# Performance work log

Hardware: AMD Instinct MI355X
Metric: run time of the kernel (lower is better)

The kernel has to match this reference:

```python
import jax, jax.numpy as jnp
import numpy as np

B, D_IN, FD = 32768, 2048, 128
N1 = N2 = N3 = 4
T = 1.0  # temperature buffer value (eval mode)
LN_EPS = 1e-5

def _gelu(x):
    return jax.nn.gelu(x, approximate=False)  # torch nn.GELU default = exact erf

def setup_inputs() -> dict:
    key = jax.random.key(0)
    ks = iter(jax.random.split(key, 64))
    def rn(shape, s=0.02):
        return jax.random.normal(next(ks), shape, jnp.float32) * s
    inp = {"x": jax.random.normal(next(ks), (B, D_IN), jnp.float32)}
    # input_proj: Linear(2048,512) GELU Linear(512,256) LayerNorm(256)
    inp.update(ipW1=rn((D_IN, 512)), ipb1=jnp.zeros(512), ipW2=rn((512, 256)), ipb2=jnp.zeros(256),
               ln_g=jnp.ones(256), ln_b=jnp.zeros(256))
    def level(din, nc, pfx):
        return {pfx+"W3d": rn((din, 3)), pfx+"b3d": jnp.zeros(3),
                pfx+"c": rn((nc, 3), 0.3), pfx+"lr": jnp.zeros(nc),
                pfx+"f1W": rn((din, FD)), pfx+"f1b": jnp.zeros(FD),
                pfx+"f2W": rn((FD, FD)), pfx+"f2b": jnp.zeros(FD),
                pfx+"rW": rn((FD+3, nc)), pfx+"rb": jnp.zeros(nc)}
    inp.update(level(256, N1, "l1"))
    inp.update(level(FD, N2, "l2"))
    inp.update(level(FD, N3, "l3"))
    # expert_head: Linear(128+4+4+4, 256) GELU Linear(256, 64)
    inp.update(ehW1=rn((FD+N1+N2+N3, 256)), ehb1=jnp.zeros(256),
               ehW2=rn((256, N1*N2*N3)), ehb2=jnp.zeros(N1*N2*N3))
    return inp

def _level_fwd(x, W3d, b3d, c, f1W, f1b, f2W, f2b, rW, rb):
    # x: (B, din) -> probs (B, nc), features (B, FD)
    pos = x @ W3d + b3d                                   # (B, 3)
    d_sq = ((pos[:, None, :] - c[None, :, :]) ** 2).sum(-1)  # (B, nc)
    geo = -d_sq / (2.0 * T * T + 1e-8)                    # non-spectral geo signal
    feat = _gelu(x @ f1W + f1b) @ f2W + f2b               # (B, FD)
    logits = jnp.concatenate([feat, pos], axis=-1) @ rW + rb + 0.5 * geo
    probs = jax.nn.softmax(logits / max(T, 0.1), axis=-1)  # eval path: plain softmax
    return probs, feat

def _router_fwd(x, ipW1, ipb1, ipW2, ipb2, ln_g, ln_b,
                l1W3d, l1b3d, l1c, l1f1W, l1f1b, l1f2W, l1f2b, l1rW, l1rb,
                l2W3d, l2b3d, l2c, l2f1W, l2f1b, l2f2W, l2f2b, l2rW, l2rb,
                l3W3d, l3b3d, l3c, l3f1W, l3f1b, l3f2W, l3f2b, l3rW, l3rb,
                ehW1, ehb1, ehW2, ehb2):
    h = _gelu(x @ ipW1 + ipb1) @ ipW2 + ipb2
    mu = h.mean(-1, keepdims=True)
    var = ((h - mu) ** 2).mean(-1, keepdims=True)
    h = (h - mu) * jax.lax.rsqrt(var + LN_EPS) * ln_g + ln_b  # LayerNorm(256)
    p1, f1 = _level_fwd(h,  l1W3d, l1b3d, l1c, l1f1W, l1f1b, l1f2W, l1f2b, l1rW, l1rb)
    p2, f2 = _level_fwd(f1, l2W3d, l2b3d, l2c, l2f1W, l2f1b, l2f2W, l2f2b, l2rW, l2rb)
    p3, f3 = _level_fwd(f2, l3W3d, l3b3d, l3c, l3f1W, l3f1b, l3f2W, l3f2b, l3rW, l3rb)
    combined = jnp.concatenate([f3, p1, p2, p3], axis=-1)  # (B, 140)
    logits = _gelu(combined @ ehW1 + ehb1) @ ehW2 + ehb2   # (B, 64)
    expert_probs = jax.nn.softmax(logits / max(T, 0.1), axis=-1)
    return expert_probs

def reference(x, ipW1, ipb1, ipW2, ipb2, ln_g, ln_b,
              l1W3d, l1b3d, l1c, l1lr, l1f1W, l1f1b, l1f2W, l1f2b, l1rW, l1rb,
              l2W3d, l2b3d, l2c, l2lr, l2f1W, l2f1b, l2f2W, l2f2b, l2rW, l2rb,
              l3W3d, l3b3d, l3c, l3lr, l3f1W, l3f1b, l3f2W, l3f2b, l3rW, l3rb,
              ehW1, ehb1, ehW2, ehb2):
    # l?lr (log_radii) are unused in non-spectral mode, matching the source.
    expert_probs = _router_fwd(x, ipW1, ipb1, ipW2, ipb2, ln_g, ln_b,
                               l1W3d, l1b3d, l1c, l1f1W, l1f1b, l1f2W, l1f2b, l1rW, l1rb,
                               l2W3d, l2b3d, l2c, l2f1W, l2f1b, l2f2W, l2f2b, l2rW, l2rb,
                               l3W3d, l3b3d, l3c, l3f1W, l3f1b, l3f2W, l3f2b, l3rW, l3rb,
                               ehW1, ehb1, ehW2, ehb2)
    expert_ids = jnp.argmax(expert_probs, axis=-1)
    return expert_probs, expert_ids
```

## Files before the change

kernel.cpp:

```cpp
#include <hip/hip_runtime.h>
#include <hip/hip_bf16.h>
#include <cstdint>
#include <cstddef>


typedef short  s8v  __attribute__((ext_vector_type(8)));
typedef float  f4v  __attribute__((ext_vector_type(4)));
typedef float  f16v __attribute__((ext_vector_type(16)));
typedef unsigned int u32;

#define B_ROWS 32768

__device__ inline short f2bf(float x) {
    __hip_bfloat16 h = __float2bfloat16(x);
    return __builtin_bit_cast(short, h);
}
__device__ inline float bf2f(short s) {
    return __bfloat162float(__builtin_bit_cast(__hip_bfloat16, s));
}
__device__ inline float gelu_f(float x) {
    return 0.5f * x * (1.0f + erff(x * 0.70710678118654752440f));
}
__device__ inline void gload_lds16(const short* g, short* l) {
    __builtin_amdgcn_global_load_lds(
        (const __attribute__((address_space(1))) u32*)g,
        (__attribute__((address_space(3))) u32*)l, 16, 0, 0);
}

__global__ void split_w1_img(const float* __restrict__ W, short* __restrict__ img)
{
    const int idx = blockIdx.x * 256 + threadIdx.x;
    const int p = idx & 7;
    const int n = (idx >> 3) & 511;
    const int t = idx >> 12;
    const int cs = p ^ (n & 7);
    const int plane = cs >> 2, kc = cs & 3;
    const int kbase = t * 32 + kc * 8;
    s8v v8;
    #pragma unroll
    for (int e = 0; e < 8; ++e) {
        const float v = W[(size_t)(kbase + e) * 512 + n];
        const short h = f2bf(v);
        v8[e] = plane ? f2bf(v - bf2f(h)) : h;
    }
    *(s8v*)&img[(size_t)((t * 512 + n) * 64 + p * 8)] = v8;
}

__launch_bounds__(256, 4)
__global__ void gemm1k(const float* __restrict__ X,
                       const short* __restrict__ Bimg,
                       const float* __restrict__ bias,
                       float* __restrict__ out)
{
    __shared__ short smem[128 * 64 * 2];
    short* Ab = smem;
    short* Bb = smem + 128 * 64;

    const int tid = threadIdx.x;
    const int l = tid & 63, wid = tid >> 6;
    const int wr = wid >> 1, wc = wid & 1;

    const int d = blockIdx.x;
    const int xcd = d & 7;
    const int m0 = ((xcd & 1) * 128 + (d >> 3)) * 128;
    const int n0 = (xcd >> 1) * 128;

    const int ar = tid & 127, ah = tid >> 7;
    const float* xP = X + (size_t)(m0 + ar) * 2048 + ah * 16;
    short* awr = Ab + ar * 64;
    const int pw0 = ((ah * 2    ) ^ (ar & 7)) * 8;
    const int pw1 = ((ah * 2 + 1) ^ (ar & 7)) * 8;
    const int pw2 = ((ah * 2 + 4) ^ (ar & 7)) * 8;
    const int pw3 = ((ah * 2 + 5) ^ (ar & 7)) * 8;

    const short* bP = Bimg + (size_t)n0 * 64 + (size_t)(wid * 4) * 512 + (size_t)l * 8;
    short* bD = Bb + wid * 4 * 512;

    f16v acc[2][2];
    #pragma unroll
    for (int m = 0; m < 2; ++m)
        #pragma unroll
        for (int n = 0; n < 2; ++n) acc[m][n] = (f16v)0.0f;

    f4v cur0, cur1, cur2, cur3;
    cur0 = *(const f4v*)(xP + 0);
    cur1 = *(const f4v*)(xP + 4);
    cur2 = *(const f4v*)(xP + 8);
    cur3 = *(const f4v*)(xP + 12);

    for (int t = 0; t < 64; ++t) {
        s8v hi0, hi1, lo0, lo1;
        #pragma unroll
        for (int e = 0; e < 4; ++e) {
            float v;
            short h;
            v = cur0[e]; h = f2bf(v); hi0[e]     = h; lo0[e]     = f2bf(v - bf2f(h));
            v = cur1[e]; h = f2bf(v); hi0[e + 4] = h; lo0[e + 4] = f2bf(v - bf2f(h));
            v = cur2[e]; h = f2bf(v); hi1[e]     = h; lo1[e]     = f2bf(v - bf2f(h));
            v = cur3[e]; h = f2bf(v); hi1[e + 4] = h; lo1[e + 4] = f2bf(v - bf2f(h));
        }
        __syncthreads();
        *(s8v*)&awr[pw0] = hi0;
        *(s8v*)&awr[pw1] = hi1;
        *(s8v*)&awr[pw2] = lo0;
        *(s8v*)&awr[pw3] = lo1;
        {
            const short* bt = bP + (size_t)t * 32768;
            gload_lds16(bt,          bD);
            gload_lds16(bt +  512,   bD + 512);
            gload_lds16(bt + 1024,   bD + 1024);
            gload_lds16(bt + 1536,   bD + 1536);
        }
        if (t < 63) {
            const float* p = xP + (t + 1) * 32;
            cur0 = *(const f4v*)(p + 0);
            cur1 = *(const f4v*)(p + 4);
            cur2 = *(const f4v*)(p + 8);
            cur3 = *(const f4v*)(p + 12);
        }
        __syncthreads();

        #pragma unroll
        for (int ks = 0; ks < 2; ++ks) {
            const int ph = (ks * 2 + (l >> 5)) ^ (l & 7);
            s8v ahf[2], alf[2], bhf[2], blf[2];
            #pragma unroll
            for (int m = 0; m < 2; ++m) {
                const int row = wr * 64 + m * 32 + (l & 31);
                ahf[m] = *(const s8v*)&Ab[row * 64 + ph * 8];
                alf[m] = *(const s8v*)&Ab[row * 64 + (ph ^ 4) * 8];
            }
            #pragma unroll
            for (int n = 0; n < 2; ++n) {
                const int col = wc * 64 + n * 32 + (l & 31);
                bhf[n] = *(const s8v*)&Bb[col * 64 + ph * 8];
                blf[n] = *(const s8v*)&Bb[col * 64 + (ph ^ 4) * 8];
            }
            #pragma unroll
            for (int m = 0; m < 2; ++m)
                #pragma unroll
                for (int n = 0; n < 2; ++n) {
                    acc[m][n] = __builtin_amdgcn_mfma_f32_32x32x16_bf16(ahf[m], bhf[n], acc[m][n], 0, 0, 0);
                    acc[m][n] = __builtin_amdgcn_mfma_f32_32x32x16_bf16(ahf[m], blf[n], acc[m][n], 0, 0, 0);
                    acc[m][n] = __builtin_amdgcn_mfma_f32_32x32x16_bf16(alf[m], bhf[n], acc[m][n], 0, 0, 0);
                }
        }
    }

    #pragma unroll
    for (int m = 0; m < 2; ++m) {
        #pragma unroll
        for (int n = 0; n < 2; ++n) {
            const int gcol = n0 + wc * 64 + n * 32 + (l & 31);
            const float bv = bias[gcol];
            #pragma unroll
            for (int r = 0; r < 16; ++r) {
                const int grow = m0 + wr * 64 + m * 32
                               + (r & 3) + 8 * (r >> 2) + 4 * (l >> 5);
                out[(size_t)grow * 512 + gcol] = gelu_f(acc[m][n][r] + bv);
            }
        }
    }
}

struct SplitDesc { const float* W; short* dst; int K, N, Kpad, blk0; };
struct SplitPack { SplitDesc d[9]; };

__global__ void split_all(SplitPack p) {
    const int bid = blockIdx.x;
    int i = 0;
    #pragma unroll
    for (int j = 1; j < 9; ++j) if (bid >= p.d[j].blk0) i = j;
    const SplitDesc& D = p.d[i];
    const int idx = (bid - D.blk0) * 256 + threadIdx.x;
    const int total = D.N * D.Kpad;
    if (idx >= total) return;
    const int n = idx / D.Kpad, k = idx - n * D.Kpad;
    const float v = (k < D.K) ? D.W[(size_t)k * D.N + n] : 0.0f;
    const short hs = f2bf(v);
    D.dst[idx] = hs;
    D.dst[total + idx] = f2bf(v - bf2f(hs));
}

template<int BM, int BN, int EPI>
__launch_bounds__(256, 2)
__global__ void gemm32(const float* __restrict__ A, int lda,
                       const short* __restrict__ Bsp, int ldb, int NK,
                       const float* __restrict__ bias, int K, int N, int ntiles,
                       float* __restrict__ out, float* __restrict__ out2)
{
    constexpr int MF  = BM / 64;
    constexpr int NFw = BN / 64;
    constexpr int BUF = (BM + BN) * 64;
    constexpr int FPT = BM / 8;
    constexpr int TPR = 32 / FPT;
    constexpr int nBI = BN / 32;
    __shared__ short smem[2 * BUF];

    const int tid = threadIdx.x;
    const int l   = tid & 63, wid = tid >> 6;
    const int wr  = wid >> 1, wc = wid & 1;
    const int bid = blockIdx.x;
    const int ntb = bid % ntiles, mtb = bid / ntiles;
    const int m0  = mtb * BM, n0 = ntb * BN;

    const int ar = tid / TPR, aseg = tid % TPR;
    const float* aP = A + (size_t)(m0 + ar) * lda + aseg * FPT;

    const short* bg[nBI];
    {
        const int cs = (l & 7) ^ (l >> 3);
        const int plane = cs >> 2, kslot = cs & 3;
        #pragma unroll
        for (int j = 0; j < nBI; ++j) {
            const int col = (wid * nBI + j) * 8 + (l >> 3);
            bg[j] = Bsp + (size_t)plane * NK + (size_t)(n0 + col) * ldb + kslot * 8;
        }
    }

    f16v acc[MF][NFw];
    #pragma unroll
    for (int m = 0; m < MF; ++m)
// ... 58 lines not shown
                }
            __builtin_amdgcn_s_setprio(0);
        }
    };

    const int NT = K / 32;
    loadA(0);
    stageB(0, smem);
    writeA(smem);
    __syncthreads();
    for (int t = 0; t < NT; ++t) {
        short* curb = smem + (t & 1) * BUF;
        short* nxtb = smem + ((t & 1) ^ 1) * BUF;
        const bool pf = (t + 1 < NT);
        if (pf) { loadA(t + 1); stageB(t + 1, nxtb); }
        compute(curb);
        if (pf) writeA(nxtb);
        __syncthreads();
    }

    if constexpr (EPI <= 1) {
        #pragma unroll
        for (int m = 0; m < MF; ++m) {
            #pragma unroll
            for (int n = 0; n < NFw; ++n) {
                const int gcol = n0 + wc * (BN / 2) + n * 32 + (l & 31);
                const float bv = bias[gcol];
                #pragma unroll
                for (int r = 0; r < 16; ++r) {
                    const int grow = m0 + wr * (BM / 2) + m * 32
                                   + (r & 3) + 8 * (r >> 2) + 4 * (l >> 5);
                    float xv = acc[m][n][r] + bv;
                    if constexpr (EPI == 0) xv = gelu_f(xv);
                    out[(size_t)grow * N + gcol] = xv;
                }
            }
        }
    } else {
        float* LT = reinterpret_cast<float*>(smem);
        const int gcolL = wc * 32 + (l & 31);
        const float bv = bias[gcolL];
        #pragma unroll
        for (int r = 0; r < 16; ++r) {
            const int row = wr * 32 + (r & 3) + 8 * (r >> 2) + 4 * (l >> 5);
            LT[row * 64 + gcolL] = acc[0][0][r] + bv;
        }
        __syncthreads();
        const int r = tid >> 2, q = tid & 3;
        const float* Lr = LT + r * 64 + q * 16;
        float mx = Lr[0];
        #pragma unroll
        for (int c = 1; c < 16; ++c) mx = fmaxf(mx, Lr[c]);
        mx = fmaxf(mx, __shfl_xor(mx, 1));
        mx = fmaxf(mx, __shfl_xor(mx, 2));
        float ev[16]; float s = 0.0f;
        #pragma unroll
        for (int c = 0; c < 16; ++c) { ev[c] = expf(Lr[c] - mx); s += ev[c]; }
        s += __shfl_xor(s, 1);
        s += __shfl_xor(s, 2);
        float pmax = -1.0f; int arg = 0;
        #pragma unroll
        for (int c = 0; c < 16; ++c) {
            const float pv = ev[c] / s;
            out[(size_t)(m0 + r) * 64 + q * 16 + c] = pv;
            if (pv > pmax) { pmax = pv; arg = q * 16 + c; }
        }
        #pragma unroll
        for (int off = 1; off <= 2; off <<= 1) {
            const float po = __shfl_xor(pmax, off);
            const int   ao = __shfl_xor(arg, off);
            if (po > pmax || (po == pmax && ao < arg)) { pmax = po; arg = ao; }
        }
        if (q == 0) out2[m0 + r] = (float)arg;
    }
}

__global__ __launch_bounds__(256) void ln_kernel(float* __restrict__ H,
                                                 const float* __restrict__ G,
                                                 const float* __restrict__ Bv)
{
    const int row = blockIdx.x * 4 + (threadIdx.x >> 6);
    const int l   = threadIdx.x & 63;
    float* hr = H + (size_t)row * 256;
    f4v v = *reinterpret_cast<const f4v*>(&hr[l * 4]);
    float s = v[0] + v[1] + v[2] + v[3];
    #pragma unroll
    for (int o = 32; o; o >>= 1) s += __shfl_xor(s, o);
    const float mu = s * 0.00390625f;
    f4v d = v - mu;
    float q = d[0]*d[0] + d[1]*d[1] + d[2]*d[2] + d[3]*d[3];
    #pragma unroll
    for (int o = 32; o; o >>= 1) q += __shfl_xor(q, o);
    const float var = q * 0.00390625f;
    const float sc  = 1.0f / sqrtf(var + 1e-5f);
    f4v gg = *reinterpret_cast<const f4v*>(&G[l * 4]);
    f4v bb = *reinterpret_cast<const f4v*>(&Bv[l * 4]);
    f4v o4 = d * sc * gg + bb;
    *reinterpret_cast<f4v*>(&hr[l * 4]) = o4;
}

__global__ __launch_bounds__(256) void p_kernel(
    const float* __restrict__ X, int din,
    const float* __restrict__ F,
    const float* __restrict__ W3d, const float* __restrict__ b3d,
    const float* __restrict__ cc,
    const float* __restrict__ rW, const float* __restrict__ rb,
    float* __restrict__ P)
{
    const int row = blockIdx.x * 4 + (threadIdx.x >> 6);
    const int l   = threadIdx.x & 63;
    float px0 = 0.f, px1 = 0.f, px2 = 0.f;
    const int per = din >> 6;
    const float* xr = X + (size_t)row * din;
    for (int i = 0; i < per; ++i) {
        const int k = l + (i << 6);
        const float xv = xr[k];
        px0 += xv * W3d[k*3 + 0];
        px1 += xv * W3d[k*3 + 1];
        px2 += xv * W3d[k*3 + 2];
    }
    float g0 = 0.f, g1 = 0.f, g2 = 0.f, g3 = 0.f;
    const float* fr = F + (size_t)row * 128;
    #pragma unroll
    for (int i = 0; i < 2; ++i) {
        const int k = l + (i << 6);
        const float fv = fr[k];
        g0 += fv * rW[k*4 + 0]; g1 += fv * rW[k*4 + 1];
        g2 += fv * rW[k*4 + 2]; g3 += fv * rW[k*4 + 3];
    }
    #pragma unroll
    for (int o = 32; o; o >>= 1) {
        px0 += __shfl_xor(px0, o); px1 += __shfl_xor(px1, o); px2 += __shfl_xor(px2, o);
        g0  += __shfl_xor(g0, o);  g1  += __shfl_xor(g1, o);
        g2  += __shfl_xor(g2, o);  g3  += __shfl_xor(g3, o);
    }
    if (l == 0) {
        const float pos0 = px0 + b3d[0], pos1 = px1 + b3d[1], pos2 = px2 + b3d[2];
        float lg[4];
        float mx = -1e30f;
        float gg[4] = {g0, g1, g2, g3};
        #pragma unroll
        for (int c = 0; c < 4; ++c) {
            float a = gg[c] + rb[c]
                    + pos0 * rW[512 + c] + pos1 * rW[516 + c] + pos2 * rW[520 + c];
            const float d0 = pos0 - cc[c*3 + 0];
            const float d1 = pos1 - cc[c*3 + 1];
            const float d2 = pos2 - cc[c*3 + 2];
            a += 0.5f * (-(d0*d0 + d1*d1 + d2*d2) / 2.00000001f);
            lg[c] = a;
            mx = fmaxf(mx, a);
        }
        const float e0 = expf(lg[0]-mx), e1 = expf(lg[1]-mx),
                    e2 = expf(lg[2]-mx), e3 = expf(lg[3]-mx);
        const float s = e0 + e1 + e2 + e3;
        float* pr = P + (size_t)row * 4;
        pr[0] = e0/s; pr[1] = e1/s; pr[2] = e2/s; pr[3] = e3/s;
    }
}

__global__ void concat_kernel(const float* __restrict__ f3,
                              const float* __restrict__ P1,
                              const float* __restrict__ P2,
                              const float* __restrict__ P3,
                              float* __restrict__ C)
{
    const int idx = blockIdx.x * 256 + threadIdx.x;
    const int row = idx / 160, j = idx - row * 160;
    float v;
    if      (j < 128) v = f3[(size_t)row * 128 + j];
    else if (j < 132) v = P1[(size_t)row * 4 + (j - 128)];
    else if (j < 136) v = P2[(size_t)row * 4 + (j - 132)];
    else if (j < 140) v = P3[(size_t)row * 4 + (j - 136)];
    else              v = 0.0f;
    C[idx] = v;
}

extern "C" void kernel_launch(void* const* d_in, const int* in_sizes, int n_in,
                              void* d_out, int out_size, void* d_ws, size_t ws_size,
                              hipStream_t stream)
{
    (void)in_sizes; (void)n_in; (void)out_size; (void)ws_size;

    const float* x    = (const float*)d_in[0];
    const float* ipW1 = (const float*)d_in[1];
    const float* ipb1 = (const float*)d_in[2];
    const float* ipW2 = (const float*)d_in[3];
    const float* ipb2 = (const float*)d_in[4];
    const float* ln_g = (const float*)d_in[5];
    const float* ln_b = (const float*)d_in[6];
    const float* W3d[3] = {(const float*)d_in[7],  (const float*)d_in[17], (const float*)d_in[27]};
    const float* b3d[3] = {(const float*)d_in[8],  (const float*)d_in[18], (const float*)d_in[28]};
    const float* cc[3]  = {(const float*)d_in[9],  (const float*)d_in[19], (const float*)d_in[29]};
    const float* f1W[3] = {(const float*)d_in[11], (const float*)d_in[21], (const float*)d_in[31]};
    const float* f1b[3] = {(const float*)d_in[12], (const float*)d_in[22], (const float*)d_in[32]};
    const float* f2W[3] = {(const float*)d_in[13], (const float*)d_in[23], (const float*)d_in[33]};
    const float* f2b[3] = {(const float*)d_in[14], (const float*)d_in[24], (const float*)d_in[34]};
    const float* rW[3]  = {(const float*)d_in[15], (const float*)d_in[25], (const float*)d_in[35]};
    const float* rb[3]  = {(const float*)d_in[16], (const float*)d_in[26], (const float*)d_in[36]};
    const float* ehW1 = (const float*)d_in[37];
    const float* ehb1 = (const float*)d_in[38];
    const float* ehW2 = (const float*)d_in[39];
    const float* ehb2 = (const float*)d_in[40];

    size_t off = 0;
    auto take = [&](size_t bytes) -> void* {
        void* p = (char*)d_ws + off;
        off += (bytes + 255) & ~(size_t)255;
        return p;
    };
    auto takeW = [&](int N, int Kpad) -> short* {
        return (short*)take((size_t)2 * N * Kpad * 2);
    };
    short* W1img = (short*)take((size_t)64 * 512 * 64 * 2);
    short* W2s = takeW(256, 512);
    short* L1a = takeW(128, 256);
    short* L1b = takeW(128, 128);
    short* L2a = takeW(128, 128);
    short* L2b = takeW(128, 128);
    short* L3a = takeW(128, 128);
    short* L3b = takeW(128, 128);
    short* E1s = takeW(256, 160);
    short* E2s = takeW(64, 256);
    float* h1 = (float*)take((size_t)B_ROWS * 512 * 4);
    float* h2 = (float*)take((size_t)B_ROWS * 256 * 4);
    float* zg = (float*)take((size_t)B_ROWS * 128 * 4);
    float* f1 = (float*)take((size_t)B_ROWS * 128 * 4);
    float* f2 = (float*)take((size_t)B_ROWS * 128 * 4);
    float* f3 = (float*)take((size_t)B_ROWS * 128 * 4);
    float* p1 = (float*)take((size_t)B_ROWS * 4 * 4);
    float* p2 = (float*)take((size_t)B_ROWS * 4 * 4);
    float* p3 = (float*)take((size_t)B_ROWS * 4 * 4);
    float* comb = h1;
    float* geh  = (float*)((char*)h1 + ((size_t)22 << 20));

    split_w1_img<<<(64 * 512 * 8) / 256, 256, 0, stream>>>(ipW1, W1img);
    SplitPack sp;
    int blk = 0;
    auto desc = [&](int i, const float* W, short* dst, int K, int N, int Kpad) {
        sp.d[i] = {W, dst, K, N, Kpad, blk};
        blk += (N * Kpad + 255) / 256;
    };
    desc(0, ipW2,   W2s,  512, 256,  512);
    desc(1, f1W[0], L1a,  256, 128,  256);
    desc(2, f2W[0], L1b,  128, 128,  128);
    desc(3, f1W[1], L2a,  128, 128,  128);
    desc(4, f2W[1], L2b,  128, 128,  128);
    desc(5, f1W[2], L3a,  128, 128,  128);
    desc(6, f2W[2], L3b,  128, 128,  128);
    desc(7, ehW1,   E1s,  140, 256,  160);
    desc(8, ehW2,   E2s,  256,  64,  256);
    split_all<<<blk, 256, 0, stream>>>(sp);

    const dim3 blkT(256);
    constexpr int MG128 = B_ROWS / 128;
    constexpr int MG64  = B_ROWS / 64;

    gemm1k<<<1024, blkT, 0, stream>>>(x, W1img, ipb1, h1);
    gemm32<128,128,1><<<MG128*2, blkT, 0, stream>>>(h1,  512, W2s,  512, 256*512,  ipb2,  512, 256, 2, h2, nullptr);
    ln_kernel<<<B_ROWS/4, 256, 0, stream>>>(h2, ln_g, ln_b);

    gemm32<64,128,0><<<MG64, blkT, 0, stream>>>(h2, 256, L1a, 256, 128*256, f1b[0], 256, 128, 1, zg, nullptr);
    gemm32<64,128,1><<<MG64, blkT, 0, stream>>>(zg, 128, L1b, 128, 128*128, f2b[0], 128, 128, 1, f1, nullptr);
    p_kernel<<<B_ROWS/4, 256, 0, stream>>>(h2, 256, f1, W3d[0], b3d[0], cc[0], rW[0], rb[0], p1);

    gemm32<64,128,0><<<MG64, blkT, 0, stream>>>(f1, 128, L2a, 128, 128*128, f1b[1], 128, 128, 1, zg, nullptr);
    gemm32<64,128,1><<<MG64, blkT, 0, stream>>>(zg, 128, L2b, 128, 128*128, f2b[1], 128, 128, 1, f2, nullptr);
    p_kernel<<<B_ROWS/4, 256, 0, stream>>>(f1, 128, f2, W3d[1], b3d[1], cc[1], rW[1], rb[1], p2);

    gemm32<64,128,0><<<MG64, blkT, 0, stream>>>(f2, 128, L3a, 128, 128*128, f1b[2], 128, 128, 1, zg, nullptr);
    gemm32<64,128,1><<<MG64, blkT, 0, stream>>>(zg, 128, L3b, 128, 128*128, f2b[2], 128, 128, 1, f3, nullptr);
    p_kernel<<<B_ROWS/4, 256, 0, stream>>>(f2, 128, f3, W3d[2], b3d[2], cc[2], rW[2], rb[2], p3);

    concat_kernel<<<(B_ROWS*160)/256, 256, 0, stream>>>(f3, p1, p2, p3, comb);
    gemm32<64,128,0><<<MG64*2, blkT, 0, stream>>>(comb, 160, E1s, 160, 256*160, ehb1, 160, 256, 2, geh, nullptr);
    gemm32<64,64,2><<<MG64, blkT, 0, stream>>>(geh, 256, E2s, 256, 64*256, ehb2, 256, 64, 1,
                                               (float*)d_out, (float*)d_out + (size_t)B_ROWS * 64);
}
```

Measured before the change: 495.0 us.

## Rewrite first GEMM with 256x256 tiles, double-buffered LDS and prefetch pipeline

Replaces the 128x128-tile, 256-thread first-layer GEMM with a 512-thread, 256x256-tile kernel. It double-buffers A and B in 128KB of dynamic LDS and loads the X tile two steps ahead, so global loads and the bf16 hi/lo split overlap the MFMA work. It also raises wave priority around the MFMA block and changes the block-to-XCD mapping. The larger tile improves data reuse and cuts the barrier per step, at the cost of one block per CU, a large register footprint and possible LDS or launch-attribute limits on dynamic shared memory.

```diff
diff --git a/kernel.cpp b/kernel.cpp
--- a/kernel.cpp
+++ b/kernel.cpp
@@ -46,116 +46,145 @@
     *(s8v*)&img[(size_t)((t * 512 + n) * 64 + p * 8)] = v8;
 }
 
-__launch_bounds__(256, 4)
-__global__ void gemm1k(const float* __restrict__ X,
-                       const short* __restrict__ Bimg,
-                       const float* __restrict__ bias,
-                       float* __restrict__ out)
-{
-    __shared__ short smem[128 * 64 * 2];
-    short* Ab = smem;
-    short* Bb = smem + 128 * 64;
+struct ARegs { f4v v[4]; };
+
+__launch_bounds__(512, 1)
+__global__ void gemmA(const float* __restrict__ X,
+                      const short* __restrict__ Bimg,
+                      const float* __restrict__ bias,
+                      float* __restrict__ out)
+{
+    extern __shared__ short smem[];
+    constexpr int NT = 64;
+    short* const buf0 = smem;
+    short* const buf1 = smem + 32768;
 
     const int tid = threadIdx.x;
     const int l = tid & 63, wid = tid >> 6;
-    const int wr = wid >> 1, wc = wid & 1;
+    const int wr = wid >> 2, wc = wid & 3;
 
     const int d = blockIdx.x;
-    const int xcd = d & 7;
-    const int m0 = ((xcd & 1) * 128 + (d >> 3)) * 128;
-    const int n0 = (xcd >> 1) * 128;
-
-    const int ar = tid & 127, ah = tid >> 7;
-    const float* xP = X + (size_t)(m0 + ar) * 2048 + ah * 16;
-    short* awr = Ab + ar * 64;
-    const int pw0 = ((ah * 2    ) ^ (ar & 7)) * 8;
-    const int pw1 = ((ah * 2 + 1) ^ (ar & 7)) * 8;
-    const int pw2 = ((ah * 2 + 4) ^ (ar & 7)) * 8;
-    const int pw3 = ((ah * 2 + 5) ^ (ar & 7)) * 8;
-
-    const short* bP = Bimg + (size_t)n0 * 64 + (size_t)(wid * 4) * 512 + (size_t)l * 8;
-    short* bD = Bb + wid * 4 * 512;
-
-    f16v acc[2][2];
-    #pragma unroll
-    for (int m = 0; m < 2; ++m)
-        #pragma unroll
-        for (int n = 0; n < 2; ++n) acc[m][n] = (f16v)0.0f;
-
-    f4v cur0, cur1, cur2, cur3;
-    cur0 = *(const f4v*)(xP + 0);
-    cur1 = *(const f4v*)(xP + 4);
-    cur2 = *(const f4v*)(xP + 8);
-    cur3 = *(const f4v*)(xP + 12);
-
-    for (int t = 0; t < 64; ++t) {
+    const int n0 = ((d >> 2) & 1) * 256;
+    const int m0 = ((d & 3) * 32 + (d >> 3)) * 256;
+
+    const int arow = tid >> 1, ahalf = tid & 1;
+    const float* xP = X + (size_t)(m0 + arow) * 2048 + ahalf * 16;
+    const int aoff = arow * 64;
+    const int ps0 = ((ahalf * 2    ) ^ (arow & 7)) * 8;
+    const int ps1 = ((ahalf * 2 + 1) ^ (arow & 7)) * 8;
+    const int ps2 = ((ahalf * 2 + 4) ^ (arow & 7)) * 8;
+    const int ps3 = ((ahalf * 2 + 5) ^ (arow & 7)) * 8;
+
+    const short* bgl = Bimg + (size_t)(n0 + wid * 32) * 64 + l * 8;
+    const int bdo = 16384 + wid * 2048;
+
+    f16v acc[4][2];
+    #pragma unroll
+    for (int m = 0; m < 4; ++m) { acc[m][0] = (f16v)0.0f; acc[m][1] = (f16v)0.0f; }
+
+    auto stageB = [&](int t, short* buf) {
+        const short* bt = bgl + (size_t)t * 32768;
+        short* bd = buf + bdo;
+        gload_lds16(bt,        bd);
+        gload_lds16(bt +  512, bd + 512);
+        gload_lds16(bt + 1024, bd + 1024);
+        gload_lds16(bt + 1536, bd + 1536);
+    };
+    auto loadA = [&](int t, ARegs& r) {
+        const float* p = xP + t * 32;
+        r.v[0] = *(const f4v*)(p);
+        r.v[1] = *(const f4v*)(p + 4);
+        r.v[2] = *(const f4v*)(p + 8);
+        r.v[3] = *(const f4v*)(p + 12);
+    };
+    auto cvtWrite = [&](const ARegs& r, short* buf) {
         s8v hi0, hi1, lo0, lo1;
         #pragma unroll
         for (int e = 0; e < 4; ++e) {
-            float v;
-            short h;
-            v = cur0[e]; h = f2bf(v); hi0[e]     = h; lo0[e]     = f2bf(v - bf2f(h));
-            v = cur1[e]; h = f2bf(v); hi0[e + 4] = h; lo0[e + 4] = f2bf(v - bf2f(h));
-            v = cur2[e]; h = f2bf(v); hi1[e]     = h; lo1[e]     = f2bf(v - bf2f(h));
-            v = cur3[e]; h = f2bf(v); hi1[e + 4] = h; lo1[e + 4] = f2bf(v - bf2f(h));
-        }
-        __syncthreads();
-        *(s8v*)&awr[pw0] = hi0;
-        *(s8v*)&awr[pw1] = hi1;
-        *(s8v*)&awr[pw2] = lo0;
-        *(s8v*)&awr[pw3] = lo1;
-        {
-            const short* bt = bP + (size_t)t * 32768;
-            gload_lds16(bt,          bD);
-            gload_lds16(bt +  512,   bD + 512);
-            gload_lds16(bt + 1024,   bD + 1024);
-            gload_lds16(bt + 1536,   bD + 1536);
-        }
-        if (t < 63) {
-            const float* p = xP + (t + 1) * 32;
-            cur0 = *(const f4v*)(p + 0);
-            cur1 = *(const f4v*)(p + 4);
-            cur2 = *(const f4v*)(p + 8);
-            cur3 = *(const f4v*)(p + 12);
-        }
-        __syncthreads();
-
+            float v; short h;
+            v = r.v[0][e]; h = f2bf(v); hi0[e]     = h; lo0[e]     = f2bf(v - bf2f(h));
+            v = r.v[1][e]; h = f2bf(v); hi0[e + 4] = h; lo0[e + 4] = f2bf(v - bf2f(h));
+            v = r.v[2][e]; h = f2bf(v); hi1[e]     = h; lo1[e]     = f2bf(v - bf2f(h));
+            v = r.v[3][e]; h = f2bf(v); hi1[e + 4] = h; lo1[e + 4] = f2bf(v - bf2f(h));
+        }
+        short* aw = buf + aoff;
+        *(s8v*)&aw[ps0] = hi0;
+        *(s8v*)&aw[ps1] = hi1;
+        *(s8v*)&aw[ps2] = lo0;
+        *(s8v*)&aw[ps3] = lo1;
+    };
+    auto compute = [&](const short* buf) {
+        const short* Ab = buf;
+        const short* Bb = buf + 16384;
         #pragma unroll
         for (int ks = 0; ks < 2; ++ks) {
-            const int ph = (ks * 2 + (l >> 5)) ^ (l & 7);
-            s8v ahf[2], alf[2], bhf[2], blf[2];
-            #pragma unroll
-            for (int m = 0; m < 2; ++m) {
-                const int row = wr * 64 + m * 32 + (l & 31);
+            const int c0 = ks * 2 + (l >> 5);
+            s8v ahf[4], alf[4], bhf[2], blf[2];
+            #pragma unroll
+            for (int m = 0; m < 4; ++m) {
+                const int row = wr * 128 + m * 32 + (l & 31);
+                const int ph = c0 ^ (row & 7);
                 ahf[m] = *(const s8v*)&Ab[row * 64 + ph * 8];
                 alf[m] = *(const s8v*)&Ab[row * 64 + (ph ^ 4) * 8];
             }
             #pragma unroll
             for (int n = 0; n < 2; ++n) {
                 const int col = wc * 64 + n * 32 + (l & 31);
+                const int ph = c0 ^ (col & 7);
                 bhf[n] = *(const s8v*)&Bb[col * 64 + ph * 8];
                 blf[n] = *(const s8v*)&Bb[col * 64 + (ph ^ 4) * 8];
             }
-            #pragma unroll
-            for (int m = 0; m < 2; ++m)
+            __builtin_amdgcn_s_setprio(1);
+            #pragma unroll
+            for (int m = 0; m < 4; ++m)
                 #pragma unroll
                 for (int n = 0; n < 2; ++n) {
                     acc[m][n] = __builtin_amdgcn_mfma_f32_32x32x16_bf16(ahf[m], bhf[n], acc[m][n], 0, 0, 0);
                     acc[m][n] = __builtin_amdgcn_mfma_f32_32x32x16_bf16(ahf[m], blf[n], acc[m][n], 0, 0, 0);
                     acc[m][n] = __builtin_amdgcn_mfma_f32_32x32x16_bf16(alf[m], bhf[n], acc[m][n], 0, 0, 0);
                 }
-        }
-    }
-
-    #pragma unroll
-    for (int m = 0; m < 2; ++m) {
+            __builtin_amdgcn_s_setprio(0);
+        }
+    };
+
+    ARegs arA, arB;
+
+    stageB(0, buf0);
+    loadA(0, arA);
+    loadA(1, arB);
+    __builtin_amdgcn_sched_barrier(0);
+    cvtWrite(arA, buf0);
+    asm volatile("s_waitcnt lgkmcnt(0)" ::: "memory");
+    __builtin_amdgcn_s_barrier();
+
+    auto body = [&](int t, short* bufC, short* bufN, ARegs& ld, ARegs& cv) {
+        const bool doStage = (t + 1 < NT);
+        if (doStage) stageB(t + 1, bufN);
+        if (t + 2 < NT) loadA(t + 2, ld);
+        __builtin_amdgcn_sched_barrier(0);
+        if (doStage) cvtWrite(cv, bufN);
+        if (t == NT - 1)
+            asm volatile("s_waitcnt vmcnt(0)" ::: "memory");
+        asm volatile("s_waitcnt lgkmcnt(0)" ::: "memory");
+        __builtin_amdgcn_s_barrier();
+        compute(bufC);
+        __builtin_amdgcn_s_barrier();
+    };
+
+    for (int tp = 0; tp < NT; tp += 2) {
+        body(tp,     buf0, buf1, arA, arB);
+        body(tp + 1, buf1, buf0, arB, arA);
+    }
+
+    #pragma unroll
+    for (int m = 0; m < 4; ++m) {
         #pragma unroll
         for (int n = 0; n < 2; ++n) {
             const int gcol = n0 + wc * 64 + n * 32 + (l & 31);
             const float bv = bias[gcol];
             #pragma unroll
             for (int r = 0; r < 16; ++r) {
-                const int grow = m0 + wr * 64 + m * 32
+                const int grow = m0 + wr * 128 + m * 32
                                + (r & 3) + 8 * (r >> 2) + 4 * (l >> 5);
                 out[(size_t)grow * 512 + gcol] = gelu_f(acc[m][n][r] + bv);
             }
@@ -535,7 +564,7 @@
     constexpr int MG128 = B_ROWS / 128;
     constexpr int MG64  = B_ROWS / 64;
 
-    gemm1k<<<1024, blkT, 0, stream>>>(x, W1img, ipb1, h1);
+    gemmA<<<256, 512, 131072, stream>>>(x, W1img, ipb1, h1);
     gemm32<128,128,1><<<MG128*2, blkT, 0, stream>>>(h1,  512, W2s,  512, 256*512,  ipb2,  512, 256, 2, h2, nullptr);
     ln_kernel<<<B_ROWS/4, 256, 0, stream>>>(h2, ln_g, ln_b);
 
```

After: 610.7 us. 23.4% more time.

## Fuse LayerNorm into GEMM epilogue, fuse level MLPs, drop concat kernel

Applied to the files above, without the earlier changes.

LayerNorm now runs in a new GEMM epilogue (EPI 3) that computes the full 256-wide row per block, which removes the separate LN pass over h2. Each level's two-layer MLP becomes one kernel, levelk, that keeps the GELU intermediate in LDS instead of writing and re-reading a global zg buffer. The last level's features and all three probability vectors are written straight into the padded 160-column combined buffer, so the concat kernel goes away. In exchange the LN GEMM uses a wider 64x256 tile, and the padding columns of the combined buffer are no longer zeroed; they rely on the zero-padded weights.

```diff
diff --git a/kernel.cpp b/kernel.cpp
--- a/kernel.cpp
+++ b/kernel.cpp
@@ -122,17 +122,19 @@
 
         #pragma unroll
         for (int ks = 0; ks < 2; ++ks) {
-            const int ph = (ks * 2 + (l >> 5)) ^ (l & 7);
+            const int ph0 = ks * 2 + (l >> 5);
             s8v ahf[2], alf[2], bhf[2], blf[2];
             #pragma unroll
             for (int m = 0; m < 2; ++m) {
                 const int row = wr * 64 + m * 32 + (l & 31);
+                const int ph = ph0 ^ (row & 7);
                 ahf[m] = *(const s8v*)&Ab[row * 64 + ph * 8];
                 alf[m] = *(const s8v*)&Ab[row * 64 + (ph ^ 4) * 8];
             }
             #pragma unroll
             for (int n = 0; n < 2; ++n) {
                 const int col = wc * 64 + n * 32 + (l & 31);
+                const int ph = ph0 ^ (col & 7);
                 bhf[n] = *(const s8v*)&Bb[col * 64 + ph * 8];
                 blf[n] = *(const s8v*)&Bb[col * 64 + (ph ^ 4) * 8];
             }
@@ -182,12 +184,148 @@
     D.dst[total + idx] = f2bf(v - bf2f(hs));
 }
 
+template<int DIN, int OSTR>
+__launch_bounds__(256, 2)
+__global__ void levelk(const float* __restrict__ X,
+                       const short* __restrict__ Wa, const float* __restrict__ ba,
+                       const short* __restrict__ Wb, const float* __restrict__ bb,
+                       float* __restrict__ F)
+{
+    constexpr int NT1 = DIN / 32;
+    __shared__ short stepb[(64 + 128) * 64];
+    __shared__ float gb[64 * 132];
+    short* Ab = stepb;
+    short* Bb = stepb + 64 * 64;
+
+    const int tid = threadIdx.x;
+    const int l = tid & 63, wid = tid >> 6;
+    const int wr = wid >> 1, wc = wid & 1;
+    const int m0 = blockIdx.x * 64;
+
+    const int ar = tid >> 2, aseg = tid & 3;
+    short* aw = Ab + ar * 64;
+    const int ps0 = ((aseg    ) ^ (ar & 7)) * 8;
+    const int ps1 = ((aseg + 4) ^ (ar & 7)) * 8;
+
+    const int cs = (l & 7) ^ (l >> 3);
+    const int bplane = cs >> 2, kslot = cs & 3;
+
+    f16v acc[2];
+    acc[0] = (f16v)0.0f; acc[1] = (f16v)0.0f;
+
+    auto computeStep = [&]() {
+        #pragma unroll
+        for (int ks = 0; ks < 2; ++ks) {
+            const int c0 = ks * 2 + (l >> 5);
+            const int row = wr * 32 + (l & 31);
+            const int pa = c0 ^ (row & 7);
+            s8v ah = *(const s8v*)&Ab[row * 64 + pa * 8];
+            s8v al = *(const s8v*)&Ab[row * 64 + (pa ^ 4) * 8];
+            #pragma unroll
+            for (int n = 0; n < 2; ++n) {
+                const int col = wc * 64 + n * 32 + (l & 31);
+                const int pb = c0 ^ (col & 7);
+                s8v bh = *(const s8v*)&Bb[col * 64 + pb * 8];
+                s8v bl = *(const s8v*)&Bb[col * 64 + (pb ^ 4) * 8];
+                acc[n] = __builtin_amdgcn_mfma_f32_32x32x16_bf16(ah, bh, acc[n], 0, 0, 0);
+                acc[n] = __builtin_amdgcn_mfma_f32_32x32x16_bf16(ah, bl, acc[n], 0, 0, 0);
+                acc[n] = __builtin_amdgcn_mfma_f32_32x32x16_bf16(al, bh, acc[n], 0, 0, 0);
+            }
+        }
+    };
+    auto cvt = [&](const f4v& u, const f4v& w, s8v& hi, s8v& lo) {
+        #pragma unroll
+        for (int e = 0; e < 4; ++e) {
+            short h;
+            h = f2bf(u[e]); hi[e]     = h; lo[e]     = f2bf(u[e] - bf2f(h));
+            h = f2bf(w[e]); hi[e + 4] = h; lo[e + 4] = f2bf(w[e] - bf2f(h));
+        }
+    };
+
+    {
+        const float* xP = X + (size_t)(m0 + ar) * DIN + aseg * 8;
+        f4v cA = *(const f4v*)(xP);
+        f4v cB = *(const f4v*)(xP + 4);
+        for (int t = 0; t < NT1; ++t) {
+            s8v hi, lo; cvt(cA, cB, hi, lo);
+            __syncthreads();
+            *(s8v*)&aw[ps0] = hi;
+            *(s8v*)&aw[ps1] = lo;
+            #pragma unroll
+            for (int j = 0; j < 4; ++j) {
+                const int col = (wid * 4 + j) * 8 + (l >> 3);
+                gload_lds16(Wa + (size_t)bplane * (128 * DIN) + (size_t)col * DIN
+                               + t * 32 + kslot * 8,
+                            Bb + (wid * 4 + j) * 512);
+            }
+            if (t + 1 < NT1) {
+                const float* p = xP + (t + 1) * 32;
+                cA = *(const f4v*)(p);
+                cB = *(const f4v*)(p + 4);
+            }
+            __syncthreads();
+            computeStep();
+        }
+    }
+
+    #pragma unroll
+    for (int n = 0; n < 2; ++n) {
+        const int col = wc * 64 + n * 32 + (l & 31);
+        const float bv = ba[col];
+        #pragma unroll
+        for (int r = 0; r < 16; ++r) {
+            const int row = wr * 32 + (r & 3) + 8 * (r >> 2) + 4 * (l >> 5);
+            gb[row * 132 + col] = gelu_f(acc[n][r] + bv);
+        }
+    }
+    acc[0] = (f16v)0.0f; acc[1] = (f16v)0.0f;
+    __syncthreads();
+
+    {
+        const float* gP = gb + ar * 132 + aseg * 8;
+        f4v cA = *(const f4v*)(gP);
+        f4v cB = *(const f4v*)(gP + 4);
+        for (int t = 0; t < 4; ++t) {
+            s8v hi, lo; cvt(cA, cB, hi, lo);
+            __syncthreads();
+            *(s8v*)&aw[ps0] = hi;
+            *(s8v*)&aw[ps1] = lo;
+            #pragma unroll
+            for (int j = 0; j < 4; ++j) {
+                const int col = (wid * 4 + j) * 8 + (l >> 3);
+                gload_lds16(Wb + (size_t)bplane * (128 * 128) + (size_t)col * 128
+                               + t * 32 + kslot * 8,
+                            Bb + (wid * 4 + j) * 512);
+            }
+            if (t + 1 < 4) {
+                const float* p = gP + (t + 1) * 32;
+                cA = *(const f4v*)(p);
+                cB = *(const f4v*)(p + 4);
+            }
+            __syncthreads();
+            computeStep();
+        }
+    }
+
+    #pragma unroll
+    for (int n = 0; n < 2; ++n) {
+        const int col = wc * 64 + n * 32 + (l & 31);
+        const float bv = bb[col];
+        #pragma unroll
+        for (int r = 0; r < 16; ++r) {
+            const int row = wr * 32 + (r & 3) + 8 * (r >> 2) + 4 * (l >> 5);
+            F[(size_t)(m0 + row) * OSTR + col] = acc[n][r] + bv;
+        }
+    }
+}
+
 template<int BM, int BN, int EPI>
 __launch_bounds__(256, 2)
 __global__ void gemm32(const float* __restrict__ A, int lda,
                        const short* __restrict__ Bsp, int ldb, int NK,
                        const float* __restrict__ bias, int K, int N, int ntiles,
-                       float* __restrict__ out, float* __restrict__ out2)
+                       float* __restrict__ out, float* __restrict__ out2,
+                       const float* __restrict__ lng, const float* __restrict__ lnb)
 {
     constexpr int MF  = BM / 64;
     constexpr int NFw = BN / 64;
@@ -316,7 +454,7 @@
                 }
             }
         }
-    } else {
+    } else if constexpr (EPI == 2) {
         float* LT = reinterpret_cast<float*>(smem);
         const int gcolL = wc * 32 + (l & 31);
         const float bv = bias[gcolL];
@@ -352,40 +490,48 @@
             if (po > pmax || (po == pmax && ao < arg)) { pmax = po; arg = ao; }
         }
         if (q == 0) out2[m0 + r] = (float)arg;
-    }
-}
-
-__global__ __launch_bounds__(256) void ln_kernel(float* __restrict__ H,
-                                                 const float* __restrict__ G,
-                                                 const float* __restrict__ Bv)
-{
-    const int row = blockIdx.x * 4 + (threadIdx.x >> 6);
-    const int l   = threadIdx.x & 63;
-    float* hr = H + (size_t)row * 256;
-    f4v v = *reinterpret_cast<const f4v*>(&hr[l * 4]);
-    float s = v[0] + v[1] + v[2] + v[3];
-    #pragma unroll
-    for (int o = 32; o; o >>= 1) s += __shfl_xor(s, o);
-    const float mu = s * 0.00390625f;
-    f4v d = v - mu;
-    float q = d[0]*d[0] + d[1]*d[1] + d[2]*d[2] + d[3]*d[3];
-    #pragma unroll
-    for (int o = 32; o; o >>= 1) q += __shfl_xor(q, o);
-    const float var = q * 0.00390625f;
-    const float sc  = 1.0f / sqrtf(var + 1e-5f);
-    f4v gg = *reinterpret_cast<const f4v*>(&G[l * 4]);
-    f4v bb = *reinterpret_cast<const f4v*>(&Bv[l * 4]);
-    f4v o4 = d * sc * gg + bb;
-    *reinterpret_cast<f4v*>(&hr[l * 4]) = o4;
+    } else {
+        float* LT = reinterpret_cast<float*>(smem);
+        #pragma unroll
+        for (int n = 0; n < NFw; ++n) {
+            const int col = wc * (BN / 2) + n * 32 + (l & 31);
+            const float bv = bias[col];
+            #pragma unroll
+            for (int r = 0; r < 16; ++r) {
+                const int row = wr * 32 + (r & 3) + 8 * (r >> 2) + 4 * (l >> 5);
+                LT[row * 264 + col] = acc[0][n][r] + bv;
+            }
+        }
+        __syncthreads();
+        const int r = tid >> 2, q = tid & 3;
+        const float* Lr = LT + r * 264 + q * 64;
+        float s = 0.0f;
+        #pragma unroll
+        for (int i = 0; i < 64; ++i) s += Lr[i];
+        s += __shfl_xor(s, 1);
+        s += __shfl_xor(s, 2);
+        const float mu = s * 0.00390625f;
+        float qv = 0.0f;
+        #pragma unroll
+        for (int i = 0; i < 64; ++i) { const float dd = Lr[i] - mu; qv += dd * dd; }
+        qv += __shfl_xor(qv, 1);
+        qv += __shfl_xor(qv, 2);
+        const float sc = 1.0f / sqrtf(qv * 0.00390625f + 1e-5f);
+        #pragma unroll
+        for (int i = 0; i < 64; ++i) {
+            const int c = q * 64 + i;
+            out[(size_t)(m0 + r) * 256 + c] = (Lr[i] - mu) * sc * lng[c] + lnb[c];
+        }
+    }
 }
 
 __global__ __launch_bounds__(256) void p_kernel(
     const float* __restrict__ X, int din,
-    const float* __restrict__ F,
+    const float* __restrict__ F, int fstr,
     const float* __restrict__ W3d, const float* __restrict__ b3d,
     const float* __restrict__ cc,
     const float* __restrict__ rW, const float* __restrict__ rb,
-    float* __restrict__ P)
+    float* __restrict__ Pout)
 {
     const int row = blockIdx.x * 4 + (threadIdx.x >> 6);
     const int l   = threadIdx.x & 63;
@@ -400,7 +546,7 @@
         px2 += xv * W3d[k*3 + 2];
     }
     float g0 = 0.f, g1 = 0.f, g2 = 0.f, g3 = 0.f;
-    const float* fr = F + (size_t)row * 128;
+    const float* fr = F + (size_t)row * fstr;
     #pragma unroll
     for (int i = 0; i < 2; ++i) {
         const int k = l + (i << 6);
@@ -433,26 +579,9 @@
         const float e0 = expf(lg[0]-mx), e1 = expf(lg[1]-mx),
                     e2 = expf(lg[2]-mx), e3 = expf(lg[3]-mx);
         const float s = e0 + e1 + e2 + e3;
-        float* pr = P + (size_t)row * 4;
+        float* pr = Pout + (size_t)row * 160;
         pr[0] = e0/s; pr[1] = e1/s; pr[2] = e2/s; pr[3] = e3/s;
     }
-}
-
-__global__ void concat_kernel(const float* __restrict__ f3,
-                              const float* __restrict__ P1,
-                              const float* __restrict__ P2,
-                              const float* __restrict__ P3,
-                              float* __restrict__ C)
-{
-    const int idx = blockIdx.x * 256 + threadIdx.x;
-    const int row = idx / 160, j = idx - row * 160;
-    float v;
-    if      (j < 128) v = f3[(size_t)row * 128 + j];
-    else if (j < 132) v = P1[(size_t)row * 4 + (j - 128)];
-    else if (j < 136) v = P2[(size_t)row * 4 + (j - 132)];
-    else if (j < 140) v = P3[(size_t)row * 4 + (j - 136)];
-    else              v = 0.0f;
-    C[idx] = v;
 }
 
 extern "C" void kernel_launch(void* const* d_in, const int* in_sizes, int n_in,
@@ -503,13 +632,8 @@
     short* E2s = takeW(64, 256);
     float* h1 = (float*)take((size_t)B_ROWS * 512 * 4);
     float* h2 = (float*)take((size_t)B_ROWS * 256 * 4);
-    float* zg = (float*)take((size_t)B_ROWS * 128 * 4);
     float* f1 = (float*)take((size_t)B_ROWS * 128 * 4);
     float* f2 = (float*)take((size_t)B_ROWS * 128 * 4);
-    float* f3 = (float*)take((size_t)B_ROWS * 128 * 4);
-    float* p1 = (float*)take((size_t)B_ROWS * 4 * 4);
-    float* p2 = (float*)take((size_t)B_ROWS * 4 * 4);
-    float* p3 = (float*)take((size_t)B_ROWS * 4 * 4);
     float* comb = h1;
     float* geh  = (float*)((char*)h1 + ((size_t)22 << 20));
 
@@ -532,27 +656,22 @@
     split_all<<<blk, 256, 0, stream>>>(sp);
 
     const dim3 blkT(256);
-    constexpr int MG128 = B_ROWS / 128;
-    constexpr int MG64  = B_ROWS / 64;
+    constexpr int MG64 = B_ROWS / 64;
 
     gemm1k<<<1024, blkT, 0, stream>>>(x, W1img, ipb1, h1);
-    gemm32<128,128,1><<<MG128*2, blkT, 0, stream>>>(h1,  512, W2s,  512, 256*512,  ipb2,  512, 256, 2, h2, nullptr);
-    ln_kernel<<<B_ROWS/4, 256, 0, stream>>>(h2, ln_g, ln_b);
-
-    gemm32<64,128,0><<<MG64, blkT, 0, stream>>>(h2, 256, L1a, 256, 128*256, f1b[0], 256, 128, 1, zg, nullptr);
-    gemm32<64,128,1><<<MG64, blkT, 0, stream>>>(zg, 128, L1b, 128, 128*128, f2b[0], 128, 128, 1, f1, nullptr);
-    p_kernel<<<B_ROWS/4, 256, 0, stream>>>(h2, 256, f1, W3d[0], b3d[0], cc[0], rW[0], rb[0], p1);
-
-    gemm32<64,128,0><<<MG64, blkT, 0, stream>>>(f1, 128, L2a, 128, 128*128, f1b[1], 128, 128, 1, zg, nullptr);
-    gemm32<64,128,1><<<MG64, blkT, 0, stream>>>(zg, 128, L2b, 128, 128*128, f2b[1], 128, 128, 1, f2, nullptr);
-    p_kernel<<<B_ROWS/4, 256, 0, stream>>>(f1, 128, f2, W3d[1], b3d[1], cc[1], rW[1], rb[1], p2);
-
-    gemm32<64,128,0><<<MG64, blkT, 0, stream>>>(f2, 128, L3a, 128, 128*128, f1b[2], 128, 128, 1, zg, nullptr);
-    gemm32<64,128,1><<<MG64, blkT, 0, stream>>>(zg, 128, L3b, 128, 128*128, f2b[2], 128, 128, 1, f3, nullptr);
-    p_kernel<<<B_ROWS/4, 256, 0, stream>>>(f2, 128, f3, W3d[2], b3d[2], cc[2], rW[2], rb[2], p3);
-
-    concat_kernel<<<(B_ROWS*160)/256, 256, 0, stream>>>(f3, p1, p2, p3, comb);
-    gemm32<64,128,0><<<MG64*2, blkT, 0, stream>>>(comb, 160, E1s, 160, 256*160, ehb1, 160, 256, 2, geh, nullptr);
-    gemm32<64,64,2><<<MG64, blkT, 0, stream>>>(geh, 256, E2s, 256, 64*256, ehb2, 256, 64, 1,
-                                               (float*)d_out, (float*)d_out + (size_t)B_ROWS * 64);
-}
+    gemm32<64,256,3><<<MG64, blkT, 0, stream>>>(h1, 512, W2s, 512, 256*512, ipb2,
+                                                512, 256, 1, h2, nullptr, ln_g, ln_b);
+
+    levelk<256,128><<<MG64, blkT, 0, stream>>>(h2, L1a, f1b[0], L1b, f2b[0], f1);
+    p_kernel<<<B_ROWS/4, 256, 0, stream>>>(h2, 256, f1, 128, W3d[0], b3d[0], cc[0], rW[0], rb[0], comb + 128);
+    levelk<128,128><<<MG64, blkT, 0, stream>>>(f1, L2a, f1b[1], L2b, f2b[1], f2);
+    p_kernel<<<B_ROWS/4, 256, 0, stream>>>(f1, 128, f2, 128, W3d[1], b3d[1], cc[1], rW[1], rb[1], comb + 132);
+    levelk<128,160><<<MG64, blkT, 0, stream>>>(f2, L3a, f1b[2], L3b, f2b[2], comb);
+    p_kernel<<<B_ROWS/4, 256, 0, stream>>>(f2, 128, comb, 160, W3d[2], b3d[2], cc[2], rW[2], rb[2], comb + 136);
+
+    gemm32<64,128,0><<<MG64*2, blkT, 0, stream>>>(comb, 160, E1s, 160, 256*160, ehb1,
+                                                  160, 256, 2, geh, nullptr, nullptr, nullptr);
+    gemm32<64,64,2><<<MG64, blkT, 0, stream>>>(geh, 256, E2s, 256, 64*256, ehb2,
+                                               256, 64, 1, (float*)d_out,
+                                               (float*)d_out + (size_t)B_ROWS * 64, nullptr, nullptr);
+}
```

Result: slower. 555.5 us (+12.2%).

## Fuse level probability heads, drop concat kernel, and remap gemm1k block tiles

Applied to the files above, without the earlier changes.

The last level's second GEMM now writes its features directly into the 160-wide combined buffer through a new output-stride parameter. The three per-level probability kernels are merged into one kernel that writes the probabilities straight into columns 128–139 of that buffer, so the separate concat pass and the intermediate p1/p2/p3 and f3 buffers go away. The first GEMM's block-to-tile mapping is changed so each XCD handles a contiguous band of M rows across all four N tiles, which is meant to improve L2 reuse of X. The padding columns 140–159 now keep stale data from h1 instead of explicit zeros, which is correct only because the matching packed weights are zero there. The LDS swizzle index in gemm1k is rewritten to use row/col bits, which is equivalent to the old lane bits.

```diff
diff --git a/kernel.cpp b/kernel.cpp
--- a/kernel.cpp
+++ b/kernel.cpp
@@ -61,9 +61,9 @@
     const int wr = wid >> 1, wc = wid & 1;
 
     const int d = blockIdx.x;
-    const int xcd = d & 7;
-    const int m0 = ((xcd & 1) * 128 + (d >> 3)) * 128;
-    const int n0 = (xcd >> 1) * 128;
+    const int xcd = d & 7, s = d >> 3;
+    const int m0 = (xcd * 32 + (s >> 2)) * 128;
+    const int n0 = (s & 3) * 128;
 
     const int ar = tid & 127, ah = tid >> 7;
     const float* xP = X + (size_t)(m0 + ar) * 2048 + ah * 16;
@@ -122,17 +122,19 @@
 
         #pragma unroll
         for (int ks = 0; ks < 2; ++ks) {
-            const int ph = (ks * 2 + (l >> 5)) ^ (l & 7);
+            const int ph0 = ks * 2 + (l >> 5);
             s8v ahf[2], alf[2], bhf[2], blf[2];
             #pragma unroll
             for (int m = 0; m < 2; ++m) {
                 const int row = wr * 64 + m * 32 + (l & 31);
+                const int ph = ph0 ^ (row & 7);
                 ahf[m] = *(const s8v*)&Ab[row * 64 + ph * 8];
                 alf[m] = *(const s8v*)&Ab[row * 64 + (ph ^ 4) * 8];
             }
             #pragma unroll
             for (int n = 0; n < 2; ++n) {
                 const int col = wc * 64 + n * 32 + (l & 31);
+                const int ph = ph0 ^ (col & 7);
                 bhf[n] = *(const s8v*)&Bb[col * 64 + ph * 8];
                 blf[n] = *(const s8v*)&Bb[col * 64 + (ph ^ 4) * 8];
             }
@@ -187,7 +189,7 @@
 __global__ void gemm32(const float* __restrict__ A, int lda,
                        const short* __restrict__ Bsp, int ldb, int NK,
                        const float* __restrict__ bias, int K, int N, int ntiles,
-                       float* __restrict__ out, float* __restrict__ out2)
+                       int ostr, float* __restrict__ out, float* __restrict__ out2)
 {
     constexpr int MF  = BM / 64;
     constexpr int NFw = BN / 64;
@@ -312,7 +314,7 @@
                                    + (r & 3) + 8 * (r >> 2) + 4 * (l >> 5);
                     float xv = acc[m][n][r] + bv;
                     if constexpr (EPI == 0) xv = gelu_f(xv);
-                    out[(size_t)grow * N + gcol] = xv;
+                    out[(size_t)grow * ostr + gcol] = xv;
                 }
             }
         }
@@ -379,16 +381,14 @@
     *reinterpret_cast<f4v*>(&hr[l * 4]) = o4;
 }
 
-__global__ __launch_bounds__(256) void p_kernel(
-    const float* __restrict__ X, int din,
-    const float* __restrict__ F,
-    const float* __restrict__ W3d, const float* __restrict__ b3d,
-    const float* __restrict__ cc,
-    const float* __restrict__ rW, const float* __restrict__ rb,
-    float* __restrict__ P)
-{
-    const int row = blockIdx.x * 4 + (threadIdx.x >> 6);
-    const int l   = threadIdx.x & 63;
+__device__ void p_head(int row, int l,
+                       const float* __restrict__ X, int din,
+                       const float* __restrict__ F, int fstr,
+                       const float* __restrict__ W3d, const float* __restrict__ b3d,
+                       const float* __restrict__ cc,
+                       const float* __restrict__ rW, const float* __restrict__ rb,
+                       float* __restrict__ dst)
+{
     float px0 = 0.f, px1 = 0.f, px2 = 0.f;
     const int per = din >> 6;
     const float* xr = X + (size_t)row * din;
@@ -400,7 +400,7 @@
         px2 += xv * W3d[k*3 + 2];
     }
     float g0 = 0.f, g1 = 0.f, g2 = 0.f, g3 = 0.f;
-    const float* fr = F + (size_t)row * 128;
+    const float* fr = F + (size_t)row * fstr;
     #pragma unroll
     for (int i = 0; i < 2; ++i) {
         const int k = l + (i << 6);
@@ -433,26 +433,24 @@
         const float e0 = expf(lg[0]-mx), e1 = expf(lg[1]-mx),
                     e2 = expf(lg[2]-mx), e3 = expf(lg[3]-mx);
         const float s = e0 + e1 + e2 + e3;
-        float* pr = P + (size_t)row * 4;
-        pr[0] = e0/s; pr[1] = e1/s; pr[2] = e2/s; pr[3] = e3/s;
-    }
-}
-
-__global__ void concat_kernel(const float* __restrict__ f3,
-                              const float* __restrict__ P1,
-                              const float* __restrict__ P2,
-                              const float* __restrict__ P3,
-                              float* __restrict__ C)
-{
-    const int idx = blockIdx.x * 256 + threadIdx.x;
-    const int row = idx / 160, j = idx - row * 160;
-    float v;
-    if      (j < 128) v = f3[(size_t)row * 128 + j];
-    else if (j < 132) v = P1[(size_t)row * 4 + (j - 128)];
-    else if (j < 136) v = P2[(size_t)row * 4 + (j - 132)];
-    else if (j < 140) v = P3[(size_t)row * 4 + (j - 136)];
-    else              v = 0.0f;
-    C[idx] = v;
+        dst[0] = e0/s; dst[1] = e1/s; dst[2] = e2/s; dst[3] = e3/s;
+    }
+}
+
+struct PAllArgs {
+    const float* h2; const float* f1; const float* f2; float* comb;
+    const float* W3d[3]; const float* b3d[3]; const float* cc[3];
+    const float* rW[3];  const float* rb[3];
+};
+
+__global__ __launch_bounds__(256) void p_all(PAllArgs A)
+{
+    const int row = blockIdx.x * 4 + (threadIdx.x >> 6);
+    const int l   = threadIdx.x & 63;
+    float* cr = A.comb + (size_t)row * 160;
+    p_head(row, l, A.h2, 256, A.f1,  128, A.W3d[0], A.b3d[0], A.cc[0], A.rW[0], A.rb[0], cr + 128);
+    p_head(row, l, A.f1, 128, A.f2,  128, A.W3d[1], A.b3d[1], A.cc[1], A.rW[1], A.rb[1], cr + 132);
+    p_head(row, l, A.f2, 128, A.comb, 160, A.W3d[2], A.b3d[2], A.cc[2], A.rW[2], A.rb[2], cr + 136);
 }
 
 extern "C" void kernel_launch(void* const* d_in, const int* in_sizes, int n_in,
@@ -501,17 +499,13 @@
     short* L3b = takeW(128, 128);
     short* E1s = takeW(256, 160);
     short* E2s = takeW(64, 256);
-    float* h1 = (float*)take((size_t)B_ROWS * 512 * 4);
-    float* h2 = (float*)take((size_t)B_ROWS * 256 * 4);
-    float* zg = (float*)take((size_t)B_ROWS * 128 * 4);
-    float* f1 = (float*)take((size_t)B_ROWS * 128 * 4);
-    float* f2 = (float*)take((size_t)B_ROWS * 128 * 4);
-    float* f3 = (float*)take((size_t)B_ROWS * 128 * 4);
-    float* p1 = (float*)take((size_t)B_ROWS * 4 * 4);
-    float* p2 = (float*)take((size_t)B_ROWS * 4 * 4);
-    float* p3 = (float*)take((size_t)B_ROWS * 4 * 4);
+    float* h1  = (float*)take((size_t)B_ROWS * 512 * 4);
+    float* h2  = (float*)take((size_t)B_ROWS * 256 * 4);
+    float* zg  = (float*)take((size_t)B_ROWS * 128 * 4);
+    float* f1  = (float*)take((size_t)B_ROWS * 128 * 4);
+    float* f2  = (float*)take((size_t)B_ROWS * 128 * 4);
+    float* geh = (float*)take((size_t)B_ROWS * 256 * 4);
     float* comb = h1;
-    float* geh  = (float*)((char*)h1 + ((size_t)22 << 20));
 
     split_w1_img<<<(64 * 512 * 8) / 256, 256, 0, stream>>>(ipW1, W1img);
     SplitPack sp;
@@ -536,23 +530,28 @@
     constexpr int MG64  = B_ROWS / 64;
 
     gemm1k<<<1024, blkT, 0, stream>>>(x, W1img, ipb1, h1);
-    gemm32<128,128,1><<<MG128*2, blkT, 0, stream>>>(h1,  512, W2s,  512, 256*512,  ipb2,  512, 256, 2, h2, nullptr);
+    gemm32<128,128,1><<<MG128*2, blkT, 0, stream>>>(h1, 512, W2s, 512, 256*512, ipb2,
+                                                    512, 256, 2, 256, h2, nullptr);
     ln_kernel<<<B_ROWS/4, 256, 0, stream>>>(h2, ln_g, ln_b);
 
-    gemm32<64,128,0><<<MG64, blkT, 0, stream>>>(h2, 256, L1a, 256, 128*256, f1b[0], 256, 128, 1, zg, nullptr);
-    gemm32<64,128,1><<<MG64, blkT, 0, stream>>>(zg, 128, L1b, 128, 128*128, f2b[0], 128, 128, 1, f1, nullptr);
-    p_kernel<<<B_ROWS/4, 256, 0, stream>>>(h2, 256, f1, W3d[0], b3d[0], cc[0], rW[0], rb[0], p1);
-
-    gemm32<64,128,0><<<MG64, blkT, 0, stream>>>(f1, 128, L2a, 128, 128*128, f1b[1], 128, 128, 1, zg, nullptr);
-    gemm32<64,128,1><<<MG64, blkT, 0, stream>>>(zg, 128, L2b, 128, 128*128, f2b[1], 128, 128, 1, f2, nullptr);
-    p_kernel<<<B_ROWS/4, 256, 0, stream>>>(f1, 128, f2, W3d[1], b3d[1], cc[1], rW[1], rb[1], p2);
-
-    gemm32<64,128,0><<<MG64, blkT, 0, stream>>>(f2, 128, L3a, 128, 128*128, f1b[2], 128, 128, 1, zg, nullptr);
-    gemm32<64,128,1><<<MG64, blkT, 0, stream>>>(zg, 128, L3b, 128, 128*128, f2b[2], 128, 128, 1, f3, nullptr);
-    p_kernel<<<B_ROWS/4, 256, 0, stream>>>(f2, 128, f3, W3d[2], b3d[2], cc[2], rW[2], rb[2], p3);
-
-    concat_kernel<<<(B_ROWS*160)/256, 256, 0, stream>>>(f3, p1, p2, p3, comb);
-    gemm32<64,128,0><<<MG64*2, blkT, 0, stream>>>(comb, 160, E1s, 160, 256*160, ehb1, 160, 256, 2, geh, nullptr);
-    gemm32<64,64,2><<<MG64, blkT, 0, stream>>>(geh, 256, E2s, 256, 64*256, ehb2, 256, 64, 1,
-                                               (float*)d_out, (float*)d_out + (size_t)B_ROWS * 64);
-}
+    gemm32<64,128,0><<<MG64, blkT, 0, stream>>>(h2, 256, L1a, 256, 128*256, f1b[0], 256, 128, 1, 128, zg, nullptr);
+    gemm32<64,128,1><<<MG64, blkT, 0, stream>>>(zg, 128, L1b, 128, 128*128, f2b[0], 128, 128, 1, 128, f1, nullptr);
+    gemm32<64,128,0><<<MG64, blkT, 0, stream>>>(f1, 128, L2a, 128, 128*128, f1b[1], 128, 128, 1, 128, zg, nullptr);
+    gemm32<64,128,1><<<MG64, blkT, 0, stream>>>(zg, 128, L2b, 128, 128*128, f2b[1], 128, 128, 1, 128, f2, nullptr);
+    gemm32<64,128,0><<<MG64, blkT, 0, stream>>>(f2, 128, L3a, 128, 128*128, f1b[2], 128, 128, 1, 128, zg, nullptr);
+    gemm32<64,128,1><<<MG64, blkT, 0, stream>>>(zg, 128, L3b, 128, 128*128, f2b[2], 128, 128, 1, 160, comb, nullptr);
+
+    PAllArgs pa;
+    pa.h2 = h2; pa.f1 = f1; pa.f2 = f2; pa.comb = comb;
+    for (int i = 0; i < 3; ++i) {
+        pa.W3d[i] = W3d[i]; pa.b3d[i] = b3d[i]; pa.cc[i] = cc[i];
+        pa.rW[i] = rW[i];   pa.rb[i] = rb[i];
+    }
+    p_all<<<B_ROWS/4, 256, 0, stream>>>(pa);
+
+    gemm32<64,128,0><<<MG64*2, blkT, 0, stream>>>(comb, 160, E1s, 160, 256*160, ehb1,
+                                                  160, 256, 2, 256, geh, nullptr);
+    gemm32<64,64,2><<<MG64, blkT, 0, stream>>>(geh, 256, E2s, 256, 64*256, ehb2,
+                                               256, 64, 1, 64, (float*)d_out,
+                                               (float*)d_out + (size_t)B_ROWS * 64);
+}
```

After: 462.2 us, median of 2. -6.6%, faster.
